# Kernel optimization log

Measured on AMD Instinct MI355X. Metric: run time of the kernel, lower is better.

The kernel has to match this reference:

```python
import jax, jax.numpy as jnp
import numpy as np

B, N, M = 4, 1024, 1024
PFD, AD, GFD = 1024, 256, 512
H, DH = 4, 64
NR, CUT = 16, 2.0
SCALE = DH ** -0.5
OFFSETS = jnp.linspace(0.0, CUT, NR)
COEFF = -0.5 / (CUT / (NR - 1)) ** 2


def _ln(x, g, b, eps=1e-5):
    mu = x.mean(-1, keepdims=True)
    var = ((x - mu) ** 2).mean(-1, keepdims=True)
    return (x - mu) / jnp.sqrt(var + eps) * g + b


def _kabsch(src, tgt, w):
    # weighted Kabsch: rotation/translation aligning src -> tgt
    w = w / (w.sum(-1, keepdims=True) + 1e-8)  # (B,N)
    cs = jnp.einsum('bn,bnc->bc', w, src)
    ct = jnp.einsum('bn,bnc->bc', w, tgt)
    sc = src - cs[:, None]
    tc = tgt - ct[:, None]
    Hm = jnp.einsum('bn,bnc,bnd->bcd', w, sc, tc)  # (B,3,3)
    U, _, Vt = jnp.linalg.svd(Hm)
    V = jnp.swapaxes(Vt, -1, -2)
    d = jnp.linalg.det(V @ jnp.swapaxes(U, -1, -2))
    D = jnp.stack([jnp.ones_like(d), jnp.ones_like(d), d], -1)  # (B,3)
    R = jnp.einsum('bij,bj,bkj->bik', V, D, U)
    t = ct - jnp.einsum('bij,bj->bi', R, cs)
    return R, t


def setup_inputs():
    key = jax.random.key(0)
    it = iter(jax.random.split(key, 48))
    nrm = lambda s, sc=1.0: jax.random.normal(next(it), s, jnp.float32) * sc
    return {
        'src_point_feats': nrm((B, N, PFD)),
        'tgt_point_feats': nrm((B, M, PFD)),
        'src_points': nrm((B, N, 3)),
        'tgt_points': nrm((B, M, 3)),
        'tgt_global': nrm((B, GFD)),
        'sfp_w': nrm((PFD, AD), 0.02), 'sfp_b': jnp.zeros((AD,)), 'sfp_g': jnp.ones((AD,)), 'sfp_bb': jnp.zeros((AD,)),
        'tfp_w': nrm((PFD, AD), 0.02), 'tfp_b': jnp.zeros((AD,)), 'tfp_g': jnp.ones((AD,)), 'tfp_bb': jnp.zeros((AD,)),
        'rbf_w': nrm((NR, H), 0.1),
        'qw': nrm((AD, AD), 0.02), 'qb': jnp.zeros((AD,)),
        'kw': nrm((AD, AD), 0.02), 'kb': jnp.zeros((AD,)),
        'vw': nrm((AD, AD), 0.02), 'vb': jnp.zeros((AD,)),
        'ow': nrm((AD, AD), 0.02), 'ob': jnp.zeros((AD,)),
        'n1_g': jnp.ones((AD,)), 'n1_b': jnp.zeros((AD,)),
        'f1_w': nrm((AD, 4 * AD), 0.02), 'f1_b': jnp.zeros((4 * AD,)),
        'f2_w': nrm((4 * AD, AD), 0.02), 'f2_b': jnp.zeros((AD,)),
        'n2_g': jnp.ones((AD,)), 'n2_b': jnp.zeros((AD,)),
        'scp_w': nrm((AD, AD), 0.02), 'scp_b': jnp.zeros((AD,)),
        'tcp_w': nrm((AD, AD), 0.02), 'tcp_b': jnp.zeros((AD,)),
        'temperature': jnp.array(0.05, jnp.float32),
        'gp_w': nrm((AD, GFD), 0.02), 'gp_b': jnp.zeros((GFD,)), 'gp_g': jnp.ones((GFD,)), 'gp_bb': jnp.zeros((GFD,)),
    }


def reference(src_point_feats, tgt_point_feats, src_points, tgt_points, tgt_global,
              sfp_w, sfp_b, sfp_g, sfp_bb, tfp_w, tfp_b, tfp_g, tfp_bb, rbf_w,
              qw, qb, kw, kb, vw, vb, ow, ob, n1_g, n1_b,
              f1_w, f1_b, f2_w, f2_b, n2_g, n2_b,
              scp_w, scp_b, tcp_w, tcp_b, temperature,
              gp_w, gp_b, gp_g, gp_bb):
    # feature projections
    src_proj = jax.nn.relu(_ln(src_point_feats @ sfp_w + sfp_b, sfp_g, sfp_bb))  # (B,N,AD)
    tgt_proj = jax.nn.relu(_ln(tgt_point_feats @ tfp_w + tfp_b, tfp_g, tfp_bb))  # (B,M,AD)
    # inter-cloud geometric bias: cdist -> gaussian RBF -> per-head linear (dist no-grad)
    d2 = ((src_points ** 2).sum(-1)[:, :, None] + (tgt_points ** 2).sum(-1)[:, None, :]
          - 2.0 * jnp.einsum('bnc,bmc->bnm', src_points, tgt_points))
    dist = jnp.sqrt(jnp.clip(d2, 0.0))  # (B,N,M)
    rbf = jnp.exp(COEFF * (dist[..., None] - OFFSETS) ** 2)  # (B,N,M,NR)
    rbf = jax.lax.stop_gradient(rbf)
    bias = jnp.einsum('bnmr,rh->bhnm', rbf, rbf_w)
    # cross attention with geo bias (pre-LN on both streams, shared LN params)
    xq = _ln(src_proj, n1_g, n1_b)
    xc = _ln(tgt_proj, n1_g, n1_b)
    q = (xq @ qw + qb).reshape(B, N, H, DH)
    k = (xc @ kw + kb).reshape(B, M, H, DH)
    v = (xc @ vw + vb).reshape(B, M, H, DH)
    logits = jnp.einsum('bnhd,bmhd->bhnm', q, k) * SCALE + bias
    p = jax.nn.softmax(logits, axis=-1)
    attn_out = jnp.einsum('bhnm,bmhd->bnhd', p, v).reshape(B, N, AD) @ ow + ob
    x = src_proj + attn_out
    # FFN block (exact GELU as in torch)
    h = _ln(x, n2_g, n2_b)
    x = x + (jax.nn.gelu(h @ f1_w + f1_b, approximate=False) @ f2_w + f2_b)
    # soft correspondences + 3-step log-domain Sinkhorn
    src_corr = x @ scp_w + scp_b
    tgt_corr = tgt_proj @ tcp_w + tcp_b
    tau = jnp.clip(temperature, 0.01, 1.0)
    logS = jnp.einsum('bnd,bmd->bnm', src_corr, tgt_corr) / tau
    for _ in range(3):
        logS = logS - jax.nn.logsumexp(logS, axis=-1, keepdims=True)
        logS = logS - jax.nn.logsumexp(logS, axis=-2, keepdims=True)
    S = jnp.exp(logS)
    tgt_corr_points = jnp.einsum('bnm,bmc->bnc', S, tgt_points)
    confidence = S.max(-1)
    R_res, t_res = _kabsch(src_points, tgt_corr_points, confidence)
    src_global_new = jax.nn.relu(_ln(x.max(1) @ gp_w + gp_b, gp_g, gp_bb))
    combined = jnp.concatenate([src_global_new, tgt_global], axis=-1)
    return R_res, t_res, combined, confidence, S
```

## Files before the change

kernel.cpp:

```cpp
#include <hip/hip_runtime.h>
#include <hip/hip_bf16.h>
#include <math.h>

constexpr int Bn  = 4;
constexpr int Nn  = 1024;
constexpr int Mmm = 1024;
constexpr int PFDc = 1024;
constexpr int ADc  = 256;
constexpr int GFDc = 512;
constexpr int Hc   = 4;
constexpr int NRc  = 16;
constexpr int NSPLIT = 32;
constexpr float COEFFc = -28.125f;
constexpr float SCALEc = 0.125f;
constexpr float STEPc  = 2.0f / 15.0f;

__device__ __forceinline__ float addf(float a, float b) { return a + b; }
__device__ __forceinline__ double addd(double a, double b) { return a + b; }

#define BLK_REDUCE_F(OP, VAR, RES) \
  red[tid] = (VAR); __syncthreads(); \
  for (int st_ = 128; st_ > 0; st_ >>= 1) { if (tid < st_) red[tid] = OP(red[tid], red[tid + st_]); __syncthreads(); } \
  (RES) = red[0]; __syncthreads();

#define BLK_REDUCE_D(OP, VAR, RES) \
  redd[tid] = (VAR); __syncthreads(); \
  for (int st_ = 128; st_ > 0; st_ >>= 1) { if (tid < st_) redd[tid] = OP(redd[tid], redd[tid + st_]); __syncthreads(); } \
  (RES) = redd[0]; __syncthreads();

__device__ __forceinline__ void g512core(
    const float* __restrict__ A, int lda, const float* __restrict__ W, int ldw,
    int kbeg, int kend, int r0, int c0, int tid,
    float As[2][16][68], float Ws[2][16][68], float acc[2][4])
{
  const int tx = tid & 15, ty = tid >> 4;
  float ra[2], rb[2];
  #pragma unroll
  for (int j = 0; j < 2; ++j) {
    int e = tid + j * 512;
    ra[j] = A[(size_t)(r0 + (e >> 4)) * lda + kbeg + (e & 15)];
    rb[j] = W[(size_t)(kbeg + (e >> 6)) * ldw + c0 + (e & 63)];
  }
  #pragma unroll
  for (int j = 0; j < 2; ++j) {
    int e = tid + j * 512;
    As[0][e & 15][e >> 4] = ra[j];
    Ws[0][e >> 6][e & 63] = rb[j];
  }
  __syncthreads();

  const int nstep = (kend - kbeg) >> 4;
  for (int s = 0; s < nstep; ++s) {
    const int cur = s & 1;
    if (s + 1 < nstep) {
      const int k0 = kbeg + ((s + 1) << 4);
      #pragma unroll
      for (int j = 0; j < 2; ++j) {
        int e = tid + j * 512;
        ra[j] = A[(size_t)(r0 + (e >> 4)) * lda + k0 + (e & 15)];
        rb[j] = W[(size_t)(k0 + (e >> 6)) * ldw + c0 + (e & 63)];
      }
    }
    #pragma unroll
    for (int kk = 0; kk < 16; ++kk) {
      float2 av = *(const float2*)&As[cur][kk][ty * 2];
      float4 wv = *(const float4*)&Ws[cur][kk][tx * 4];
      float a[2] = {av.x, av.y};
      float w[4] = {wv.x, wv.y, wv.z, wv.w};
      #pragma unroll
      for (int i = 0; i < 2; ++i)
        #pragma unroll
        for (int j = 0; j < 4; ++j)
          acc[i][j] = fmaf(a[i], w[j], acc[i][j]);
    }
    if (s + 1 < nstep) {
      #pragma unroll
      for (int j = 0; j < 2; ++j) {
        int e = tid + j * 512;
        As[cur ^ 1][e & 15][e >> 4] = ra[j];
        Ws[cur ^ 1][e >> 6][e & 63] = rb[j];
      }
    }
    __syncthreads();
  }
}

__global__ __launch_bounds__(512) void gemm512_k(
    const float* __restrict__ A, const float* __restrict__ W, const float* __restrict__ bias,
    const float* __restrict__ addsrc, float* __restrict__ C,
    int K, int Cc, int act)
{
  __shared__ __align__(16) float As[2][16][68];
  __shared__ __align__(16) float Ws[2][16][68];
  const int tid = threadIdx.x;
  const int tx = tid & 15, ty = tid >> 4;
  const int r0 = blockIdx.y * 64, c0 = blockIdx.x * 64;
  float acc[2][4] = {};
  g512core(A, K, W, Cc, 0, K, r0, c0, tid, As, Ws, acc);
  #pragma unroll
  for (int i = 0; i < 2; ++i) {
    int r = r0 + ty * 2 + i;
    #pragma unroll
    for (int j = 0; j < 4; ++j) {
      int c = c0 + tx * 4 + j;
      float v = acc[i][j] + bias[c];
      if (addsrc) v += addsrc[(size_t)r * Cc + c];
      if (act == 1) v = 0.5f * v * (1.f + erff(v * 0.70710678118654752f));
      C[(size_t)r * Cc + c] = v;
    }
  }
}

__global__ __launch_bounds__(512) void gemm_sk512_k(
    const float* __restrict__ A, const float* __restrict__ W, float* __restrict__ P)
{
  __shared__ __align__(16) float As[2][16][68];
  __shared__ __align__(16) float Ws[2][16][68];
  const int tid = threadIdx.x;
  const int tx = tid & 15, ty = tid >> 4;
  const int r0 = blockIdx.y * 64, c0 = blockIdx.x * 64;
  const int koff = blockIdx.z * 256;
  float acc[2][4] = {};
  g512core(A, 1024, W, 256, koff, koff + 256, r0, c0, tid, As, Ws, acc);
  float* Pz = P + (size_t)blockIdx.z * 1048576;
  #pragma unroll
  for (int i = 0; i < 2; ++i) {
    int r = r0 + ty * 2 + i;
    #pragma unroll
    for (int j = 0; j < 4; ++j)
      Pz[(size_t)r * 256 + c0 + tx * 4 + j] = acc[i][j];
  }
}

__global__ __launch_bounds__(512) void gemm_corr2_k(
    const float* __restrict__ A0, const float* __restrict__ W0, const float* __restrict__ b0,
    float* __restrict__ C0,
    const float* __restrict__ A1, const float* __restrict__ W1, const float* __restrict__ b1,
    float* __restrict__ C1)
{
  __shared__ __align__(16) float As[2][16][68];
  __shared__ __align__(16) float Ws[2][16][68];
  const int tid = threadIdx.x;
  const int tx = tid & 15, ty = tid >> 4;
  const int r0 = blockIdx.y * 64, c0 = blockIdx.x * 64;
  const float* A = blockIdx.z ? A1 : A0;
  const float* W = blockIdx.z ? W1 : W0;
  const float* bias = blockIdx.z ? b1 : b0;
  float* C = blockIdx.z ? C1 : C0;
  float acc[2][4] = {};
  g512core(A, 256, W, 256, 0, 256, r0, c0, tid, As, Ws, acc);
  #pragma unroll
  for (int i = 0; i < 2; ++i) {
    int r = r0 + ty * 2 + i;
    #pragma unroll
    for (int j = 0; j < 4; ++j) {
      int c = c0 + tx * 4 + j;
      C[(size_t)r * 256 + c] = acc[i][j] + bias[c];
    }
  }
}

__global__ __launch_bounds__(256) void gemm_k(
    const float* __restrict__ A, const float* __restrict__ W, const float* __restrict__ bias,
    const float* __restrict__ addsrc, float* __restrict__ C,
    int R, int K, int Cc, int act)
{
  __shared__ __align__(16) float As[16][68];
  __shared__ __align__(16) float Ws[16][68];
  const int tid = threadIdx.x;
  const int tx = tid & 15, ty = tid >> 4;
  const int r0 = blockIdx.y * 64, c0 = blockIdx.x * 64;
  float acc[4][4] = {};
  for (int k0 = 0; k0 < K; k0 += 16) {
    #pragma unroll
    for (int j = 0; j < 4; ++j) {
      int e = tid + j * 256;
      int ar = e >> 4, ak = e & 15;
      int gr = r0 + ar;
      As[ak][ar] = (gr < R) ? A[(size_t)gr * K + k0 + ak] : 0.f;
    }
    #pragma unroll
    for (int j = 0; j < 4; ++j) {
      int e = tid + j * 256;
      int wk = e >> 6, wc = e & 63;
      int gc = c0 + wc;
      Ws[wk][wc] = (gc < Cc) ? W[(size_t)(k0 + wk) * Cc + gc] : 0.f;
    }
    __syncthreads();
    #pragma unroll
    for (int kk = 0; kk < 16; ++kk) {
      float4 av = *(const float4*)&As[kk][ty * 4];
      float4 wv = *(const float4*)&Ws[kk][tx * 4];
      float a[4] = {av.x, av.y, av.z, av.w};
      float w[4] = {wv.x, wv.y, wv.z, wv.w};
      #pragma unroll
      for (int i = 0; i < 4; ++i)
        #pragma unroll
        for (int j = 0; j < 4; ++j)
          acc[i][j] = fmaf(a[i], w[j], acc[i][j]);
    }
    __syncthreads();
  }
  #pragma unroll
  for (int i = 0; i < 4; ++i) {
    int r = r0 + ty * 4 + i;
    if (r >= R) continue;
    #pragma unroll
    for (int j = 0; j < 4; ++j) {
      int c = c0 + tx * 4 + j;
      if (c >= Cc) continue;
      float v = acc[i][j] + bias[c];
      if (addsrc) v += addsrc[(size_t)r * Cc + c];
      if (act == 1) v = 0.5f * v * (1.f + erff(v * 0.70710678118654752f));
      C[(size_t)r * Cc + c] = v;
    }
  }
}

__global__ __launch_bounds__(256) void gemm256_k(
    const float* __restrict__ A, const float* __restrict__ W, const float* __restrict__ bias,
    const float* __restrict__ addsrc, float* __restrict__ C,
    int R, int K, int Cc, int act)
{
  __shared__ __align__(16) float As[2][16][68];
  __shared__ __align__(16) float Ws[2][16][68];
  const int tid = threadIdx.x;
  const int tx = tid & 15, ty = tid >> 4;
  const int r0 = blockIdx.y * 64, c0 = blockIdx.x * 64;
  float acc[4][4] = {};
  float ra[4], rb[4];

  #pragma unroll
  for (int j = 0; j < 4; ++j) {
    int e = tid + j * 256;
    ra[j] = A[(size_t)(r0 + (e >> 4)) * K + (e & 15)];
    rb[j] = W[(size_t)(e >> 6) * Cc + c0 + (e & 63)];
  }
  #pragma unroll
  for (int j = 0; j < 4; ++j) {
    int e = tid + j * 256;
    As[0][e & 15][e >> 4] = ra[j];
    Ws[0][e >> 6][e & 63] = rb[j];
  }
  __syncthreads();

  const int nstep = K >> 4;
  for (int s = 0; s < nstep; ++s) {
    const int cur = s & 1;
    if (s + 1 < nstep) {
      const int k0 = (s + 1) << 4;
      #pragma unroll
      for (int j = 0; j < 4; ++j) {
        int e = tid + j * 256;
        ra[j] = A[(size_t)(r0 + (e >> 4)) * K + k0 + (e & 15)];
        rb[j] = W[(size_t)(k0 + (e >> 6)) * Cc + c0 + (e & 63)];
      }
    }
    #pragma unroll
    for (int kk = 0; kk < 16; ++kk) {
      float4 av = *(const float4*)&As[cur][kk][ty * 4];
      float4 wv = *(const float4*)&Ws[cur][kk][tx * 4];
      float a[4] = {av.x, av.y, av.z, av.w};
      float w[4] = {wv.x, wv.y, wv.z, wv.w};
      #pragma unroll
      for (int i = 0; i < 4; ++i)
        #pragma unroll
        for (int j = 0; j < 4; ++j)
          acc[i][j] = fmaf(a[i], w[j], acc[i][j]);
    }
    if (s + 1 < nstep) {
      #pragma unroll
      for (int j = 0; j < 4; ++j) {
        int e = tid + j * 256;
        As[cur ^ 1][e & 15][e >> 4] = ra[j];
        Ws[cur ^ 1][e >> 6][e & 63] = rb[j];
      }
    }
    __syncthreads();
  }
  #pragma unroll
  for (int i = 0; i < 4; ++i) {
    int r = r0 + ty * 4 + i;
    #pragma unroll
    for (int j = 0; j < 4; ++j) {
      int c = c0 + tx * 4 + j;
      float v = acc[i][j] + bias[c];
      if (addsrc) v += addsrc[(size_t)r * Cc + c];
      if (act == 1) v = 0.5f * v * (1.f + erff(v * 0.70710678118654752f));
      C[(size_t)r * Cc + c] = v;
    }
  }
}

__global__ __launch_bounds__(256) void ln4_k(
    const float* __restrict__ p, const float* __restrict__ bias,
    const float* __restrict__ g, const float* __restrict__ bb,
    float* __restrict__ out, int relu)
{
  const int row = blockIdx.x;
  const int tid = threadIdx.x;
  size_t o = (size_t)row * 256 + tid;
  float x = p[o] + p[o + 1048576] + p[o + 2097152] + p[o + 3145728] + bias[tid];
  float s = x, s2 = x * x;
  #pragma unroll
  for (int off = 32; off > 0; off >>= 1) {
    s  += __shfl_xor(s, off, 64);
    s2 += __shfl_xor(s2, off, 64);
  }
  __shared__ float as_[4], as2_[4];
  const int wv = tid >> 6, ln = tid & 63;
  if (ln == 0) { as_[wv] = s; as2_[wv] = s2; }
  __syncthreads();
  s  = as_[0] + as_[1] + as_[2] + as_[3];
  s2 = as2_[0] + as2_[1] + as2_[2] + as2_[3];
  float mu = s * (1.f / 256.f);
  float var = fmaxf(s2 * (1.f / 256.f) - mu * mu, 0.f);
  float inv = 1.f / sqrtf(var + 1e-5f);
  float v = (x - mu) * inv * g[tid] + bb[tid];
  if (relu) v = fmaxf(v, 0.f);
  out[o] = v;
}

__global__ __launch_bounds__(256) void red4_k(
    const float* __restrict__ p, const float* __restrict__ bias, float* __restrict__ out)
{
  size_t i = (size_t)blockIdx.x * 256 + threadIdx.x;
  out[i] += p[i] + p[i + 1048576] + p[i + 2097152] + p[i + 3145728] + bias[threadIdx.x];
}

__global__ __launch_bounds__(256) void pack_kv_k(
    const float* __restrict__ kw, const float* __restrict__ kb,
    const float* __restrict__ vw, const float* __restrict__ vb,
    float* __restrict__ kvw, float* __restrict__ kvb)
{
  int i = blockIdx.x * 256 + threadIdx.x;
  if (i < 256 * 512) {
    int r = i >> 9, c = i & 511;
    kvw[i] = (c < 256) ? kw[r * 256 + c] : vw[r * 256 + (c - 256)];
  } else if (i < 256 * 512 + 512) {
    int c = i - 256 * 512;
    kvb[c] = (c < 256) ? kb[c] : vb[c - 256];
  }
}

__global__ __launch_bounds__(256) void gemm_nt256_k(
    const float* __restrict__ A, const float* __restrict__ Bm, float* __restrict__ C,
    const float* __restrict__ temp)
{
  const int K = ADc;
  __shared__ __align__(16) float As[2][16][68];
  __shared__ __align__(16) float Bs[2][16][68];
  const int tid = threadIdx.x;
  const int tx = tid & 15, ty = tid >> 4;
  const int b = blockIdx.z;
  const int r0 = blockIdx.y * 64, c0 = blockIdx.x * 64;
  const float* Ab = A + (size_t)b * Nn * K;
  const float* Bb = Bm + (size_t)b * Mmm * K;
  float* Cb = C + (size_t)b * Nn * Mmm;
  float tau = fminf(fmaxf(temp[0], 0.01f), 1.0f);
  float inv_tau = 1.f / tau;
  float acc[4][4] = {};
  float ra[4], rb[4];

  #pragma unroll
  for (int j = 0; j < 4; ++j) {
    int e = tid + j * 256;
    ra[j] = Ab[(size_t)(r0 + (e >> 4)) * K + (e & 15)];
    rb[j] = Bb[(size_t)(c0 + (e >> 4)) * K + (e & 15)];
  }
  #pragma unroll
  for (int j = 0; j < 4; ++j) {
    int e = tid + j * 256;
    As[0][e & 15][e >> 4] = ra[j];
    Bs[0][e & 15][e >> 4] = rb[j];
  }
  __syncthreads();

  for (int s = 0; s < 16; ++s) {
    const int cur = s & 1;
    if (s + 1 < 16) {
      const int k0 = (s + 1) << 4;
      #pragma unroll
      for (int j = 0; j < 4; ++j) {
        int e = tid + j * 256;
        ra[j] = Ab[(size_t)(r0 + (e >> 4)) * K + k0 + (e & 15)];
        rb[j] = Bb[(size_t)(c0 + (e >> 4)) * K + k0 + (e & 15)];
      }
    }
    #pragma unroll
    for (int kk = 0; kk < 16; ++kk) {
      float4 av = *(const float4*)&As[cur][kk][ty * 4];
      float4 wv = *(const float4*)&Bs[cur][kk][tx * 4];
      float a[4] = {av.x, av.y, av.z, av.w};
      float w[4] = {wv.x, wv.y, wv.z, wv.w};
      #pragma unroll
      for (int i = 0; i < 4; ++i)
        #pragma unroll
        for (int j = 0; j < 4; ++j)
          acc[i][j] = fmaf(a[i], w[j], acc[i][j]);
    }
    if (s + 1 < 16) {
      #pragma unroll
      for (int j = 0; j < 4; ++j) {
        int e = tid + j * 256;
        As[cur ^ 1][e & 15][e >> 4] = ra[j];
        Bs[cur ^ 1][e & 15][e >> 4] = rb[j];
      }
    }
    __syncthreads();
  }
  #pragma unroll
  for (int i = 0; i < 4; ++i) {
    int r = r0 + ty * 4 + i;
    #pragma unroll
    for (int j = 0; j < 4; ++j) {
      int c = c0 + tx * 4 + j;
      Cb[(size_t)r * Mmm + c] = acc[i][j] * inv_tau;
    }
  }
}

__global__ __launch_bounds__(256) void ln_k(
    const float* __restrict__ in, const float* __restrict__ g, const float* __restrict__ bb,
    float* __restrict__ out, int Cc, int relu)
{
  const int tid = threadIdx.x;
  const int row = blockIdx.x;
  const float* x = in + (size_t)row * Cc;
  float* o = out + (size_t)row * Cc;
  __shared__ float red[256];
  float s = 0.f;
  for (int j = tid; j < Cc; j += 256) s += x[j];
  float tot; BLK_REDUCE_F(addf, s, tot);
  float mu = tot / Cc;
  float s2 = 0.f;
  for (int j = tid; j < Cc; j += 256) { float d = x[j] - mu; s2 += d * d; }
  float tot2; BLK_REDUCE_F(addf, s2, tot2);
  float inv = 1.f / sqrtf(tot2 / Cc + 1e-5f);
  for (int j = tid; j < Cc; j += 256) {
    float v = (x[j] - mu) * inv * g[j] + bb[j];
    if (relu) v = fmaxf(v, 0.f);
    o[j] = v;
  }
}

__device__ __forceinline__ void ln2_body(
    const float* __restrict__ in, const float* __restrict__ g, const float* __restrict__ bb,
    float* __restrict__ out, int row, int tid, int relu)
{
  float x = in[(size_t)row * 256 + tid];
  float s = x, s2 = x * x;
  #pragma unroll
  for (int off = 32; off > 0; off >>= 1) {
    s  += __shfl_xor(s, off, 64);
    s2 += __shfl_xor(s2, off, 64);
  }
  __shared__ float as_[4], as2_[4];
  const int wv = tid >> 6, ln = tid & 63;
  if (ln == 0) { as_[wv] = s; as2_[wv] = s2; }
  __syncthreads();
  s  = as_[0] + as_[1] + as_[2] + as_[3];
  s2 = as2_[0] + as2_[1] + as2_[2] + as2_[3];
  float mu = s * (1.f / 256.f);
  float var = fmaxf(s2 * (1.f / 256.f) - mu * mu, 0.f);
  float inv = 1.f / sqrtf(var + 1e-5f);
  float v = (x - mu) * inv * g[tid] + bb[tid];
  if (relu) v = fmaxf(v, 0.f);
  out[(size_t)row * 256 + tid] = v;
}

__global__ __launch_bounds__(256) void ln2_k(
    const float* __restrict__ in, const float* __restrict__ g, const float* __restrict__ bb,
    float* __restrict__ out, int relu)
{
  ln2_body(in, g, bb, out, blockIdx.x, threadIdx.x, relu);
}

__global__ __launch_bounds__(256) void ln2x2_k(
    const float* __restrict__ in0, float* __restrict__ out0,
    const float* __restrict__ in1, float* __restrict__ out1,
    const float* __restrict__ g, const float* __restrict__ bb)
{
  const int row = blockIdx.x;
  if (row < Bn * Nn) ln2_body(in0, g, bb, out0, row, threadIdx.x, 0);
  else               ln2_body(in1, g, bb, out1, row - Bn * Nn, threadIdx.x, 0);
}

__global__ __launch_bounds__(256) void fattn(
    const float* __restrict__ q, const float* __restrict__ kv,
    const float* __restrict__ src_pts, const float* __restrict__ tgt_pts,
    const float* __restrict__ rbfw, float* __restrict__ ctx)
{
  const int bh = blockIdx.x;
  const int b = bh >> 2, h = bh & 3;
  const int n0 = blockIdx.y * 32;
  const int tid = threadIdx.x;
  const int tx = tid & 15, ty = tid >> 4;
  const int lane = tid & 63, w = tid >> 6;
  const int mml = lane >> 4;
  const int dd  = lane & 15;

  __shared__ __align__(16) float Qs[64][36];
  __shared__ __align__(16) float Ks[64][68];
  __shared__ __align__(16) float Vs[64][68];
  __shared__ __align__(16) float Ps[32][68];
  __shared__ float spx[32], spy[32], spz[32];
  __shared__ float tpx[64], tpy[64], tpz[64];
  __shared__ float rw[16];
  __shared__ __align__(8) float2 Tb[2048];

  if (tid < 16) rw[tid] = rbfw[tid * Hc + h];
  #pragma unroll
  for (int c = 0; c < 8; ++c) {
    int n = c * 4 + mml;
    int d = w * 16 + dd;
    Qs[d][n] = q[((size_t)b * Nn + n0 + n) * ADc + h * 64 + d];
  }
  if (tid < 32) {
    spx[tid] = src_pts[((size_t)b * Nn + n0 + tid) * 3 + 0];
    spy[tid] = src_pts[((size_t)b * Nn + n0 + tid) * 3 + 1];
    spz[tid] = src_pts[((size_t)b * Nn + n0 + tid) * 3 + 2];
  }
  __syncthreads();

  for (int i = tid; i < 2048; i += 256) {
    float di = (float)i * (1.0f / 512.0f);
    float s0 = 0.f, s1 = 0.f;
    #pragma unroll
    for (int r = 0; r < NRc; ++r) {
      float dq0 = di - STEPc * r;
      float dq1 = dq0 + (1.0f / 512.0f);
      s0 = fmaf(__expf(COEFFc * dq0 * dq0), rw[r], s0);
      s1 = fmaf(__expf(COEFFc * dq1 * dq1), rw[r], s1);
    }
    Tb[i] = make_float2(s0, s1 - s0);
  }

  float kreg[16], vreg[16];
  float tp0 = 0.f, tp1 = 0.f, tp2 = 0.f;
  {
    const size_t kb_ = ((size_t)b * Mmm) * 512 + h * 64;
    #pragma unroll
    for (int c = 0; c < 16; ++c) {
      kreg[c] = kv[kb_ + (size_t)(c * 4 + mml) * 512 + w * 16 + dd];
      vreg[c] = kv[kb_ + (size_t)(c * 4 + w) * 512 + 256 + lane];
    }
    if (tid < 64) {
      tp0 = tgt_pts[((size_t)b * Mmm + tid) * 3 + 0];
      tp1 = tgt_pts[((size_t)b * Mmm + tid) * 3 + 1];
      tp2 = tgt_pts[((size_t)b * Mmm + tid) * 3 + 2];
    }
  }

  float O[2][4] = {};
  float mrun[2] = {-1e30f, -1e30f};
  float lrun[2] = {0.f, 0.f};

  for (int t = 0; t < Mmm / 64; ++t) {
    __syncthreads();
    #pragma unroll
    for (int c = 0; c < 16; ++c) Ks[w * 16 + dd][c * 4 + mml] = kreg[c];
    #pragma unroll
    for (int c = 0; c < 16; ++c) Vs[c * 4 + w][lane] = vreg[c];
    if (tid < 64) { tpx[tid] = tp0; tpy[tid] = tp1; tpz[tid] = tp2; }
    if (t + 1 < Mmm / 64) {
      const size_t kb_ = ((size_t)b * Mmm + (t + 1) * 64) * 512 + h * 64;
      #pragma unroll
      for (int c = 0; c < 16; ++c) {
        kreg[c] = kv[kb_ + (size_t)(c * 4 + mml) * 512 + w * 16 + dd];
        vreg[c] = kv[kb_ + (size_t)(c * 4 + w) * 512 + 256 + lane];
      }
// ... 305 lines not shown
  for (int r = 0; r < 3; ++r) { vv[0][r] = V[r][i0]; vv[1][r] = V[r][i1]; vv[2][r] = V[r][i2]; }
  double sg[3] = { sqrt(fmax(lam[i0], 0.0)), sqrt(fmax(lam[i1], 0.0)), sqrt(fmax(lam[i2], 0.0)) };

  double uu[3][3];
  double eps = 1e-12 * (sg[0] > 0 ? sg[0] : 1.0);
  if (sg[0] > eps) {
    for (int r = 0; r < 3; ++r)
      uu[0][r] = (A[r][0] * vv[0][0] + A[r][1] * vv[0][1] + A[r][2] * vv[0][2]) / sg[0];
    double n = sqrt(uu[0][0]*uu[0][0] + uu[0][1]*uu[0][1] + uu[0][2]*uu[0][2]);
    if (n > 1e-14) { uu[0][0]/=n; uu[0][1]/=n; uu[0][2]/=n; }
  } else { uu[0][0]=1; uu[0][1]=0; uu[0][2]=0; }
  if (sg[1] > eps) {
    for (int r = 0; r < 3; ++r)
      uu[1][r] = (A[r][0] * vv[1][0] + A[r][1] * vv[1][1] + A[r][2] * vv[1][2]) / sg[1];
  } else {
    int ax = (fabs(uu[0][0]) <= fabs(uu[0][1]) && fabs(uu[0][0]) <= fabs(uu[0][2])) ? 0
           : (fabs(uu[0][1]) <= fabs(uu[0][2]) ? 1 : 2);
    uu[1][0] = uu[1][1] = uu[1][2] = 0.0; uu[1][ax] = 1.0;
  }
  {
    double pr = uu[0][0]*uu[1][0] + uu[0][1]*uu[1][1] + uu[0][2]*uu[1][2];
    for (int r = 0; r < 3; ++r) uu[1][r] -= pr * uu[0][r];
    double n = sqrt(uu[1][0]*uu[1][0] + uu[1][1]*uu[1][1] + uu[1][2]*uu[1][2]);
    if (n > 1e-14) { uu[1][0]/=n; uu[1][1]/=n; uu[1][2]/=n; }
  }
  if (sg[2] > eps) {
    for (int r = 0; r < 3; ++r)
      uu[2][r] = (A[r][0] * vv[2][0] + A[r][1] * vv[2][1] + A[r][2] * vv[2][2]) / sg[2];
    double p0 = uu[0][0]*uu[2][0] + uu[0][1]*uu[2][1] + uu[0][2]*uu[2][2];
    double p1 = uu[1][0]*uu[2][0] + uu[1][1]*uu[2][1] + uu[1][2]*uu[2][2];
    for (int r = 0; r < 3; ++r) uu[2][r] -= p0 * uu[0][r] + p1 * uu[1][r];
    double n = sqrt(uu[2][0]*uu[2][0] + uu[2][1]*uu[2][1] + uu[2][2]*uu[2][2]);
    if (n > 1e-14) { uu[2][0]/=n; uu[2][1]/=n; uu[2][2]/=n; }
    else {
      uu[2][0] = uu[0][1]*uu[1][2] - uu[0][2]*uu[1][1];
      uu[2][1] = uu[0][2]*uu[1][0] - uu[0][0]*uu[1][2];
      uu[2][2] = uu[0][0]*uu[1][1] - uu[0][1]*uu[1][0];
    }
  } else {
    uu[2][0] = uu[0][1]*uu[1][2] - uu[0][2]*uu[1][1];
    uu[2][1] = uu[0][2]*uu[1][0] - uu[0][0]*uu[1][2];
    uu[2][2] = uu[0][0]*uu[1][1] - uu[0][1]*uu[1][0];
  }

  double detU = trip(uu[0], uu[1], uu[2]);
  double detV = trip(vv[0], vv[1], vv[2]);
  double d = (detU * detV < 0.0) ? -1.0 : 1.0;

  double R[3][3];
  for (int i = 0; i < 3; ++i)
    for (int j = 0; j < 3; ++j)
      R[i][j] = vv[0][i] * uu[0][j] + vv[1][i] * uu[1][j] + d * vv[2][i] * uu[2][j];
  for (int i = 0; i < 3; ++i) {
    double t = ct[i] - (R[i][0] * cs[0] + R[i][1] * cs[1] + R[i][2] * cs[2]);
    outT[(size_t)b * 3 + i] = (float)t;
    for (int j = 0; j < 3; ++j)
      outR[(size_t)b * 9 + i * 3 + j] = (float)R[i][j];
  }
}

__global__ __launch_bounds__(256) void xmax_part_k(const float* __restrict__ x, float* __restrict__ part)
{
  const int b = blockIdx.x, ch = blockIdx.y;
  const int d = threadIdx.x;
  float mx = -1e30f;
  const int n0 = ch * 64;
  for (int n = n0; n < n0 + 64; ++n)
    mx = fmaxf(mx, x[((size_t)b * Nn + n) * ADc + d]);
  part[((size_t)b * 16 + ch) * ADc + d] = mx;
}

__global__ __launch_bounds__(256) void xmax_comb_k(const float* __restrict__ part, float* __restrict__ xmax)
{
  const int b = blockIdx.x, d = threadIdx.x;
  float mx = -1e30f;
  for (int c = 0; c < 16; ++c) mx = fmaxf(mx, part[((size_t)b * 16 + c) * ADc + d]);
  xmax[(size_t)b * ADc + d] = mx;
}

__global__ __launch_bounds__(256) void combined_k(
    const float* __restrict__ gl, const float* __restrict__ tgt_global, float* __restrict__ outC)
{
  int i = blockIdx.x * 256 + threadIdx.x;
  int b = i >> 10, j = i & 1023;
  float v = (j < GFDc) ? gl[(size_t)b * GFDc + j] : tgt_global[(size_t)b * GFDc + (j - GFDc)];
  outC[i] = v;
}

extern "C" void kernel_launch(void* const* d_in, const int* in_sizes, int n_in,
                              void* d_out, int out_size, void* d_ws, size_t ws_size,
                              hipStream_t stream) {
  (void)in_sizes; (void)n_in; (void)out_size; (void)ws_size;
  const float* src_feats = (const float*)d_in[0];
  const float* tgt_feats = (const float*)d_in[1];
  const float* src_pts   = (const float*)d_in[2];
  const float* tgt_pts   = (const float*)d_in[3];
  const float* tgt_glob  = (const float*)d_in[4];
  const float* sfp_w = (const float*)d_in[5];  const float* sfp_b = (const float*)d_in[6];
  const float* sfp_g = (const float*)d_in[7];  const float* sfp_bb = (const float*)d_in[8];
  const float* tfp_w = (const float*)d_in[9];  const float* tfp_b = (const float*)d_in[10];
  const float* tfp_g = (const float*)d_in[11]; const float* tfp_bb = (const float*)d_in[12];
  const float* rbf_w = (const float*)d_in[13];
  const float* qw = (const float*)d_in[14]; const float* qb = (const float*)d_in[15];
  const float* kw = (const float*)d_in[16]; const float* kb = (const float*)d_in[17];
  const float* vw = (const float*)d_in[18]; const float* vb = (const float*)d_in[19];
  const float* ow = (const float*)d_in[20]; const float* ob = (const float*)d_in[21];
  const float* n1_g = (const float*)d_in[22]; const float* n1_b = (const float*)d_in[23];
  const float* f1_w = (const float*)d_in[24]; const float* f1_b = (const float*)d_in[25];
  const float* f2_w = (const float*)d_in[26]; const float* f2_b = (const float*)d_in[27];
  const float* n2_g = (const float*)d_in[28]; const float* n2_b = (const float*)d_in[29];
  const float* scp_w = (const float*)d_in[30]; const float* scp_b = (const float*)d_in[31];
  const float* tcp_w = (const float*)d_in[32]; const float* tcp_b = (const float*)d_in[33];
  const float* temp  = (const float*)d_in[34];
  const float* gp_w = (const float*)d_in[35]; const float* gp_b = (const float*)d_in[36];
  const float* gp_g = (const float*)d_in[37]; const float* gp_bb = (const float*)d_in[38];

  float* out = (float*)d_out;
  float* outR    = out;
  float* outT    = out + 36;
  float* outC    = out + 48;
  float* outConf = out + 48 + 4096;
  float* outS    = out + 48 + 4096 + 4096;

  float* ws = (float*)d_ws;
  const size_t M1 = 1048576;
  float* A_   = ws + 0 * M1;
  float* B_   = ws + 1 * M1;
  float* C_   = ws + 2 * M1;
  float* D_   = ws + 3 * M1;
  float* E_   = ws + 4 * M1;
  float* F_   = ws + 5 * M1;
  float* G_   = ws + 6 * M1;
  float* logS = ws + 0 * M1;
  float* hid  = ws + 1 * M1;
  float* tail = ws + 7 * M1;
  float* colLse = tail;
  float* pmax   = colLse + 4096;
  float* psum   = pmax + 131072;
  float* conf   = psum + 131072;
  float* tcp    = conf + 4096;
  float* xmax   = tcp + 12288;
  float* glraw  = xmax + 1024;
  float* gl     = glraw + 2048;
  double* kab   = (double*)(gl + 2048);
  float* xpart  = (float*)(kab + 64);
  float* Rn     = xpart + 16384;
  float* kvw    = pmax;
  float* kvb    = psum;

  const int BN = Bn * Nn;

  pack_kv_k<<<514, 256, 0, stream>>>(kw, kb, vw, vb, kvw, kvb);

  gemm_sk512_k<<<dim3(4, 64, 4), 512, 0, stream>>>(src_feats, sfp_w, outS);
  ln4_k<<<BN, 256, 0, stream>>>(outS, sfp_b, sfp_g, sfp_bb, G_, 1);
  gemm_sk512_k<<<dim3(4, 64, 4), 512, 0, stream>>>(tgt_feats, tfp_w, outS);
  ln4_k<<<BN, 256, 0, stream>>>(outS, tfp_b, tfp_g, tfp_bb, F_, 1);

  ln2x2_k<<<2 * BN, 256, 0, stream>>>(G_, A_, F_, B_, n1_g, n1_b);
  gemm512_k<<<dim3(4, 64), 512, 0, stream>>>(A_, qw, qb, nullptr, C_, ADc, ADc, 0);
  gemm512_k<<<dim3(8, 64), 512, 0, stream>>>(B_, kvw, kvb, nullptr, D_, ADc, 512, 0);

  fattn<<<dim3(Bn * Hc, Nn / 32), 256, 0, stream>>>(C_, D_, src_pts, tgt_pts, rbf_w, B_);
  gemm512_k<<<dim3(4, 64), 512, 0, stream>>>(B_, ow, ob, G_, G_, ADc, ADc, 0);

  ln2_k<<<BN, 256, 0, stream>>>(G_, n2_g, n2_b, A_, 0);
  gemm256_k<<<dim3(16, 64), 256, 0, stream>>>(A_, f1_w, f1_b, nullptr, hid, BN, ADc, 1024, 1);
  gemm_sk512_k<<<dim3(4, 64, 4), 512, 0, stream>>>(hid, f2_w, outS);
  red4_k<<<BN, 256, 0, stream>>>(outS, f2_b, G_);

  gemm_corr2_k<<<dim3(4, 64, 2), 512, 0, stream>>>(G_, scp_w, scp_b, E_,
                                                   F_, tcp_w, tcp_b, outS);
  gemm_nt256_k<<<dim3(16, 16, Bn), 256, 0, stream>>>(E_, outS, logS, temp);

  for (int it = 0; it < 3; ++it) {
    row_lse3_k<<<BN, 256, 0, stream>>>(logS, it == 0 ? nullptr : colLse, Rn);
    col_part2_k<<<dim3(Mmm / 256, NSPLIT, Bn), 256, 0, stream>>>(logS, Rn, pmax, psum);
    col_comb_k<<<dim3(Mmm / 256, Bn), 256, 0, stream>>>(pmax, psum, colLse);
  }
  finalize2_k<<<BN, 256, 0, stream>>>(logS, Rn, colLse, tgt_pts, outS, outConf, conf, tcp);

  kabsch_red_k<<<Bn, 256, 0, stream>>>(conf, src_pts, tcp, kab);
  kabsch_svd_k<<<1, 64, 0, stream>>>(kab, outR, outT);

  xmax_part_k<<<dim3(Bn, 16), 256, 0, stream>>>(G_, xpart);
  xmax_comb_k<<<Bn, 256, 0, stream>>>(xpart, xmax);
  gemm_k<<<dim3(GFDc / 64, 1), 256, 0, stream>>>(xmax, gp_w, gp_b, nullptr, glraw, Bn, ADc, GFDc, 0);
  ln_k<<<Bn, 256, 0, stream>>>(glraw, gp_g, gp_bb, gl, GFDc, 1);
  combined_k<<<(Bn * 2 * GFDc) / 256, 256, 0, stream>>>(gl, tgt_glob, outC);
}
```

Before: 741.8 us.

## Use 128x128 register-blocked tiles for large GEMMs and fuse the dual projections

Replaces the 64x64 tiled GEMMs used for the feature projections, the FFN and the similarity matrix with 128x128 tiles, where each of 512 threads computes an 8x4 output block. This raises arithmetic intensity per shared-memory load and cuts global reloads. The src and tgt split-K projections now run as one launch, and their LayerNorm reductions are also merged into one kernel, using the hid buffer as scratch. The cost is fewer blocks per GEMM (128-256), which may underfill the GPU's compute units, plus higher register pressure.

```diff
diff --git a/kernel.cpp b/kernel.cpp
--- a/kernel.cpp
+++ b/kernel.cpp
@@ -28,6 +28,213 @@
   for (int st_ = 128; st_ > 0; st_ >>= 1) { if (tid < st_) redd[tid] = OP(redd[tid], redd[tid + st_]); __syncthreads(); } \
   (RES) = redd[0]; __syncthreads();
 
+__device__ __forceinline__ void g128core(
+    const float* __restrict__ A, int lda, const float* __restrict__ W, int ldw,
+    int kbeg, int kend, int r0, int c0, int tid,
+    float As[2][8][132], float Ws[2][8][132], float acc[8][4])
+{
+  const int tx = tid & 31, ty = tid >> 5;
+  float ra[2], rb[2];
+  #pragma unroll
+  for (int j = 0; j < 2; ++j) {
+    int e = tid + j * 512;
+    ra[j] = A[(size_t)(r0 + (e >> 3)) * lda + kbeg + (e & 7)];
+    rb[j] = W[(size_t)(kbeg + (e >> 7)) * ldw + c0 + (e & 127)];
+  }
+  #pragma unroll
+  for (int j = 0; j < 2; ++j) {
+    int e = tid + j * 512;
+    As[0][e & 7][e >> 3] = ra[j];
+    Ws[0][e >> 7][e & 127] = rb[j];
+  }
+  __syncthreads();
+
+  const int nstep = (kend - kbeg) >> 3;
+  for (int s = 0; s < nstep; ++s) {
+    const int cur = s & 1;
+    if (s + 1 < nstep) {
+      const int k0 = kbeg + ((s + 1) << 3);
+      #pragma unroll
+      for (int j = 0; j < 2; ++j) {
+        int e = tid + j * 512;
+        ra[j] = A[(size_t)(r0 + (e >> 3)) * lda + k0 + (e & 7)];
+        rb[j] = W[(size_t)(k0 + (e >> 7)) * ldw + c0 + (e & 127)];
+      }
+    }
+    #pragma unroll
+    for (int kk = 0; kk < 8; ++kk) {
+      float4 a0 = *(const float4*)&As[cur][kk][ty * 4];
+      float4 a1 = *(const float4*)&As[cur][kk][64 + ty * 4];
+      float2 w0 = *(const float2*)&Ws[cur][kk][tx * 2];
+      float2 w1 = *(const float2*)&Ws[cur][kk][64 + tx * 2];
+      float a[8] = {a0.x, a0.y, a0.z, a0.w, a1.x, a1.y, a1.z, a1.w};
+      float w[4] = {w0.x, w0.y, w1.x, w1.y};
+      #pragma unroll
+      for (int i = 0; i < 8; ++i)
+        #pragma unroll
+        for (int j = 0; j < 4; ++j)
+          acc[i][j] = fmaf(a[i], w[j], acc[i][j]);
+    }
+    if (s + 1 < nstep) {
+      #pragma unroll
+      for (int j = 0; j < 2; ++j) {
+        int e = tid + j * 512;
+        As[cur ^ 1][e & 7][e >> 3] = ra[j];
+        Ws[cur ^ 1][e >> 7][e & 127] = rb[j];
+      }
+    }
+    __syncthreads();
+  }
+}
+
+__device__ __forceinline__ int g128row(int i, int ty) { return (i < 4) ? ty * 4 + i : 64 + ty * 4 + (i - 4); }
+__device__ __forceinline__ int g128col(int j, int tx) { return (j < 2) ? tx * 2 + j : 64 + tx * 2 + (j - 2); }
+
+__global__ __launch_bounds__(512) void gemm128_k(
+    const float* __restrict__ A, const float* __restrict__ W, const float* __restrict__ bias,
+    float* __restrict__ C, int K, int Cc, int act)
+{
+  __shared__ __align__(16) float As[2][8][132];
+  __shared__ __align__(16) float Ws[2][8][132];
+  const int tid = threadIdx.x;
+  const int tx = tid & 31, ty = tid >> 5;
+  const int r0 = blockIdx.y * 128, c0 = blockIdx.x * 128;
+  float acc[8][4] = {};
+  g128core(A, K, W, Cc, 0, K, r0, c0, tid, As, Ws, acc);
+  #pragma unroll
+  for (int i = 0; i < 8; ++i) {
+    int r = r0 + g128row(i, ty);
+    #pragma unroll
+    for (int j = 0; j < 4; ++j) {
+      int c = c0 + g128col(j, tx);
+      float v = acc[i][j] + bias[c];
+      if (act == 1) v = 0.5f * v * (1.f + erff(v * 0.70710678118654752f));
+      C[(size_t)r * Cc + c] = v;
+    }
+  }
+}
+
+__global__ __launch_bounds__(512) void gemm128sk_k(
+    const float* __restrict__ A, const float* __restrict__ W, float* __restrict__ P)
+{
+  __shared__ __align__(16) float As[2][8][132];
+  __shared__ __align__(16) float Ws[2][8][132];
+  const int tid = threadIdx.x;
+  const int tx = tid & 31, ty = tid >> 5;
+  const int r0 = blockIdx.y * 128, c0 = blockIdx.x * 128;
+  const int koff = blockIdx.z * 256;
+  float acc[8][4] = {};
+  g128core(A, 1024, W, 256, koff, koff + 256, r0, c0, tid, As, Ws, acc);
+  float* Pz = P + (size_t)blockIdx.z * 1048576;
+  #pragma unroll
+  for (int i = 0; i < 8; ++i) {
+    int r = r0 + g128row(i, ty);
+    #pragma unroll
+    for (int j = 0; j < 4; ++j)
+      Pz[(size_t)r * 256 + c0 + g128col(j, tx)] = acc[i][j];
+  }
+}
+
+__global__ __launch_bounds__(512) void proj2sk_k(
+    const float* __restrict__ srcf, const float* __restrict__ sfw,
+    const float* __restrict__ tgtf, const float* __restrict__ tfw,
+    float* __restrict__ Psrc, float* __restrict__ Ptgt)
+{
+  __shared__ __align__(16) float As[2][8][132];
+  __shared__ __align__(16) float Ws[2][8][132];
+  const int tid = threadIdx.x;
+  const int tx = tid & 31, ty = tid >> 5;
+  const int z = blockIdx.z;
+  const float* A = (z < 4) ? srcf : tgtf;
+  const float* W = (z < 4) ? sfw : tfw;
+  float* P = ((z < 4) ? Psrc : Ptgt) + (size_t)(z & 3) * 1048576;
+  const int r0 = blockIdx.y * 128, c0 = blockIdx.x * 128;
+  const int koff = (z & 3) * 256;
+  float acc[8][4] = {};
+  g128core(A, 1024, W, 256, koff, koff + 256, r0, c0, tid, As, Ws, acc);
+  #pragma unroll
+  for (int i = 0; i < 8; ++i) {
+    int r = r0 + g128row(i, ty);
+    #pragma unroll
+    for (int j = 0; j < 4; ++j)
+      P[(size_t)r * 256 + c0 + g128col(j, tx)] = acc[i][j];
+  }
+}
+
+__global__ __launch_bounds__(512) void gemm128nt_k(
+    const float* __restrict__ A, const float* __restrict__ Bm, float* __restrict__ C,
+    const float* __restrict__ temp)
+{
+  __shared__ __align__(16) float As[2][8][132];
+  __shared__ __align__(16) float Bs[2][8][132];
+  const int tid = threadIdx.x;
+  const int tx = tid & 31, ty = tid >> 5;
+  const int b = blockIdx.z;
+  const int r0 = blockIdx.y * 128, c0 = blockIdx.x * 128;
+  const float* Ab = A + (size_t)b * Nn * ADc;
+  const float* Bb = Bm + (size_t)b * Mmm * ADc;
+  float* Cb = C + (size_t)b * Nn * Mmm;
+  float tau = fminf(fmaxf(temp[0], 0.01f), 1.0f);
+  float inv_tau = 1.f / tau;
+  float acc[8][4] = {};
+  float ra[2], rb[2];
+  #pragma unroll
+  for (int j = 0; j < 2; ++j) {
+    int e = tid + j * 512;
+    ra[j] = Ab[(size_t)(r0 + (e >> 3)) * ADc + (e & 7)];
+    rb[j] = Bb[(size_t)(c0 + (e >> 3)) * ADc + (e & 7)];
+  }
+  #pragma unroll
+  for (int j = 0; j < 2; ++j) {
+    int e = tid + j * 512;
+    As[0][e & 7][e >> 3] = ra[j];
+    Bs[0][e & 7][e >> 3] = rb[j];
+  }
+  __syncthreads();
+  for (int s = 0; s < 32; ++s) {
+    const int cur = s & 1;
+    if (s + 1 < 32) {
+      const int k0 = (s + 1) << 3;
+      #pragma unroll
+      for (int j = 0; j < 2; ++j) {
+        int e = tid + j * 512;
+        ra[j] = Ab[(size_t)(r0 + (e >> 3)) * ADc + k0 + (e & 7)];
+        rb[j] = Bb[(size_t)(c0 + (e >> 3)) * ADc + k0 + (e & 7)];
+      }
+    }
+    #pragma unroll
+    for (int kk = 0; kk < 8; ++kk) {
+      float4 a0 = *(const float4*)&As[cur][kk][ty * 4];
+      float4 a1 = *(const float4*)&As[cur][kk][64 + ty * 4];
+      float2 w0 = *(const float2*)&Bs[cur][kk][tx * 2];
+      float2 w1 = *(const float2*)&Bs[cur][kk][64 + tx * 2];
+      float a[8] = {a0.x, a0.y, a0.z, a0.w, a1.x, a1.y, a1.z, a1.w};
+      float w[4] = {w0.x, w0.y, w1.x, w1.y};
+      #pragma unroll
+      for (int i = 0; i < 8; ++i)
+        #pragma unroll
+        for (int j = 0; j < 4; ++j)
+          acc[i][j] = fmaf(a[i], w[j], acc[i][j]);
+    }
+    if (s + 1 < 32) {
+      #pragma unroll
+      for (int j = 0; j < 2; ++j) {
+        int e = tid + j * 512;
+        As[cur ^ 1][e & 7][e >> 3] = ra[j];
+        Bs[cur ^ 1][e & 7][e >> 3] = rb[j];
+      }
+    }
+    __syncthreads();
+  }
+  #pragma unroll
+  for (int i = 0; i < 8; ++i) {
+    int r = r0 + g128row(i, ty);
+    #pragma unroll
+    for (int j = 0; j < 4; ++j)
+      Cb[(size_t)r * Mmm + c0 + g128col(j, tx)] = acc[i][j] * inv_tau;
+  }
+}
+
 __device__ __forceinline__ void g512core(
     const float* __restrict__ A, int lda, const float* __restrict__ W, int ldw,
     int kbeg, int kend, int r0, int c0, int tid,
@@ -108,27 +315,6 @@
       if (act == 1) v = 0.5f * v * (1.f + erff(v * 0.70710678118654752f));
       C[(size_t)r * Cc + c] = v;
     }
-  }
-}
-
-__global__ __launch_bounds__(512) void gemm_sk512_k(
-    const float* __restrict__ A, const float* __restrict__ W, float* __restrict__ P)
-{
-  __shared__ __align__(16) float As[2][16][68];
-  __shared__ __align__(16) float Ws[2][16][68];
-  const int tid = threadIdx.x;
-  const int tx = tid & 15, ty = tid >> 4;
-  const int r0 = blockIdx.y * 64, c0 = blockIdx.x * 64;
-  const int koff = blockIdx.z * 256;
-  float acc[2][4] = {};
-  g512core(A, 1024, W, 256, koff, koff + 256, r0, c0, tid, As, Ws, acc);
-  float* Pz = P + (size_t)blockIdx.z * 1048576;
-  #pragma unroll
-  for (int i = 0; i < 2; ++i) {
-    int r = r0 + ty * 2 + i;
-    #pragma unroll
-    for (int j = 0; j < 4; ++j)
-      Pz[(size_t)r * 256 + c0 + tx * 4 + j] = acc[i][j];
   }
 }
 
@@ -217,88 +403,11 @@
   }
 }
 
-__global__ __launch_bounds__(256) void gemm256_k(
-    const float* __restrict__ A, const float* __restrict__ W, const float* __restrict__ bias,
-    const float* __restrict__ addsrc, float* __restrict__ C,
-    int R, int K, int Cc, int act)
-{
-  __shared__ __align__(16) float As[2][16][68];
-  __shared__ __align__(16) float Ws[2][16][68];
-  const int tid = threadIdx.x;
-  const int tx = tid & 15, ty = tid >> 4;
-  const int r0 = blockIdx.y * 64, c0 = blockIdx.x * 64;
-  float acc[4][4] = {};
-  float ra[4], rb[4];
-
-  #pragma unroll
-  for (int j = 0; j < 4; ++j) {
-    int e = tid + j * 256;
-    ra[j] = A[(size_t)(r0 + (e >> 4)) * K + (e & 15)];
-    rb[j] = W[(size_t)(e >> 6) * Cc + c0 + (e & 63)];
-  }
-  #pragma unroll
-  for (int j = 0; j < 4; ++j) {
-    int e = tid + j * 256;
-    As[0][e & 15][e >> 4] = ra[j];
-    Ws[0][e >> 6][e & 63] = rb[j];
-  }
-  __syncthreads();
-
-  const int nstep = K >> 4;
-  for (int s = 0; s < nstep; ++s) {
-    const int cur = s & 1;
-    if (s + 1 < nstep) {
-      const int k0 = (s + 1) << 4;
-      #pragma unroll
-      for (int j = 0; j < 4; ++j) {
-        int e = tid + j * 256;
-        ra[j] = A[(size_t)(r0 + (e >> 4)) * K + k0 + (e & 15)];
-        rb[j] = W[(size_t)(k0 + (e >> 6)) * Cc + c0 + (e & 63)];
-      }
-    }
-    #pragma unroll
-    for (int kk = 0; kk < 16; ++kk) {
-      float4 av = *(const float4*)&As[cur][kk][ty * 4];
-      float4 wv = *(const float4*)&Ws[cur][kk][tx * 4];
-      float a[4] = {av.x, av.y, av.z, av.w};
-      float w[4] = {wv.x, wv.y, wv.z, wv.w};
-      #pragma unroll
-      for (int i = 0; i < 4; ++i)
-        #pragma unroll
-        for (int j = 0; j < 4; ++j)
-          acc[i][j] = fmaf(a[i], w[j], acc[i][j]);
-    }
-    if (s + 1 < nstep) {
-      #pragma unroll
-      for (int j = 0; j < 4; ++j) {
-        int e = tid + j * 256;
-        As[cur ^ 1][e & 15][e >> 4] = ra[j];
-        Ws[cur ^ 1][e >> 6][e & 63] = rb[j];
-      }
-    }
-    __syncthreads();
-  }
-  #pragma unroll
-  for (int i = 0; i < 4; ++i) {
-    int r = r0 + ty * 4 + i;
-    #pragma unroll
-    for (int j = 0; j < 4; ++j) {
-      int c = c0 + tx * 4 + j;
-      float v = acc[i][j] + bias[c];
-      if (addsrc) v += addsrc[(size_t)r * Cc + c];
-      if (act == 1) v = 0.5f * v * (1.f + erff(v * 0.70710678118654752f));
-      C[(size_t)r * Cc + c] = v;
-    }
-  }
-}
-
-__global__ __launch_bounds__(256) void ln4_k(
+__device__ __forceinline__ void ln4_body(
     const float* __restrict__ p, const float* __restrict__ bias,
     const float* __restrict__ g, const float* __restrict__ bb,
-    float* __restrict__ out, int relu)
-{
-  const int row = blockIdx.x;
-  const int tid = threadIdx.x;
+    float* __restrict__ out, int row, int tid)
+{
   size_t o = (size_t)row * 256 + tid;
   float x = p[o] + p[o + 1048576] + p[o + 2097152] + p[o + 3145728] + bias[tid];
   float s = x, s2 = x * x;
@@ -317,8 +426,18 @@
   float var = fmaxf(s2 * (1.f / 256.f) - mu * mu, 0.f);
   float inv = 1.f / sqrtf(var + 1e-5f);
   float v = (x - mu) * inv * g[tid] + bb[tid];
-  if (relu) v = fmaxf(v, 0.f);
-  out[o] = v;
+  out[o] = fmaxf(v, 0.f);
+}
+
+__global__ __launch_bounds__(256) void ln4x2_k(
+    const float* __restrict__ p0, const float* __restrict__ b0,
+    const float* __restrict__ g0, const float* __restrict__ bb0, float* __restrict__ o0,
+    const float* __restrict__ p1, const float* __restrict__ b1,
+    const float* __restrict__ g1, const float* __restrict__ bb1, float* __restrict__ o1)
+{
+  const int row = blockIdx.x;
+  if (row < Bn * Nn) ln4_body(p0, b0, g0, bb0, o0, row, threadIdx.x);
+  else               ln4_body(p1, b1, g1, bb1, o1, row - Bn * Nn, threadIdx.x);
 }
 
 __global__ __launch_bounds__(256) void red4_k(
@@ -340,83 +459,6 @@
   } else if (i < 256 * 512 + 512) {
     int c = i - 256 * 512;
     kvb[c] = (c < 256) ? kb[c] : vb[c - 256];
-  }
-}
-
-__global__ __launch_bounds__(256) void gemm_nt256_k(
-    const float* __restrict__ A, const float* __restrict__ Bm, float* __restrict__ C,
-    const float* __restrict__ temp)
-{
-  const int K = ADc;
-  __shared__ __align__(16) float As[2][16][68];
-  __shared__ __align__(16) float Bs[2][16][68];
-  const int tid = threadIdx.x;
-  const int tx = tid & 15, ty = tid >> 4;
-  const int b = blockIdx.z;
-  const int r0 = blockIdx.y * 64, c0 = blockIdx.x * 64;
-  const float* Ab = A + (size_t)b * Nn * K;
-  const float* Bb = Bm + (size_t)b * Mmm * K;
-  float* Cb = C + (size_t)b * Nn * Mmm;
-  float tau = fminf(fmaxf(temp[0], 0.01f), 1.0f);
-  float inv_tau = 1.f / tau;
-  float acc[4][4] = {};
-  float ra[4], rb[4];
-
-  #pragma unroll
-  for (int j = 0; j < 4; ++j) {
-    int e = tid + j * 256;
-    ra[j] = Ab[(size_t)(r0 + (e >> 4)) * K + (e & 15)];
-    rb[j] = Bb[(size_t)(c0 + (e >> 4)) * K + (e & 15)];
-  }
-  #pragma unroll
-  for (int j = 0; j < 4; ++j) {
-    int e = tid + j * 256;
-    As[0][e & 15][e >> 4] = ra[j];
-    Bs[0][e & 15][e >> 4] = rb[j];
-  }
-  __syncthreads();
-
-  for (int s = 0; s < 16; ++s) {
-    const int cur = s & 1;
-    if (s + 1 < 16) {
-      const int k0 = (s + 1) << 4;
-      #pragma unroll
-      for (int j = 0; j < 4; ++j) {
-        int e = tid + j * 256;
-        ra[j] = Ab[(size_t)(r0 + (e >> 4)) * K + k0 + (e & 15)];
-        rb[j] = Bb[(size_t)(c0 + (e >> 4)) * K + k0 + (e & 15)];
-      }
-    }
-    #pragma unroll
-    for (int kk = 0; kk < 16; ++kk) {
-      float4 av = *(const float4*)&As[cur][kk][ty * 4];
-      float4 wv = *(const float4*)&Bs[cur][kk][tx * 4];
-      float a[4] = {av.x, av.y, av.z, av.w};
-      float w[4] = {wv.x, wv.y, wv.z, wv.w};
-      #pragma unroll
-      for (int i = 0; i < 4; ++i)
-        #pragma unroll
-        for (int j = 0; j < 4; ++j)
-          acc[i][j] = fmaf(a[i], w[j], acc[i][j]);
-    }
-    if (s + 1 < 16) {
-      #pragma unroll
-      for (int j = 0; j < 4; ++j) {
-        int e = tid + j * 256;
-        As[cur ^ 1][e & 15][e >> 4] = ra[j];
-        Bs[cur ^ 1][e & 15][e >> 4] = rb[j];
-      }
-    }
-    __syncthreads();
-  }
-  #pragma unroll
-  for (int i = 0; i < 4; ++i) {
-    int r = r0 + ty * 4 + i;
-    #pragma unroll
-    for (int j = 0; j < 4; ++j) {
-      int c = c0 + tx * 4 + j;
-      Cb[(size_t)r * Mmm + c] = acc[i][j] * inv_tau;
-    }
   }
 }
 
@@ -1028,10 +1070,9 @@
 
   pack_kv_k<<<514, 256, 0, stream>>>(kw, kb, vw, vb, kvw, kvb);
 
-  gemm_sk512_k<<<dim3(4, 64, 4), 512, 0, stream>>>(src_feats, sfp_w, outS);
-  ln4_k<<<BN, 256, 0, stream>>>(outS, sfp_b, sfp_g, sfp_bb, G_, 1);
-  gemm_sk512_k<<<dim3(4, 64, 4), 512, 0, stream>>>(tgt_feats, tfp_w, outS);
-  ln4_k<<<BN, 256, 0, stream>>>(outS, tfp_b, tfp_g, tfp_bb, F_, 1);
+  proj2sk_k<<<dim3(2, 32, 8), 512, 0, stream>>>(src_feats, sfp_w, tgt_feats, tfp_w, outS, hid);
+  ln4x2_k<<<2 * BN, 256, 0, stream>>>(outS, sfp_b, sfp_g, sfp_bb, G_,
+                                      hid, tfp_b, tfp_g, tfp_bb, F_);
 
   ln2x2_k<<<2 * BN, 256, 0, stream>>>(G_, A_, F_, B_, n1_g, n1_b);
   gemm512_k<<<dim3(4, 64), 512, 0, stream>>>(A_, qw, qb, nullptr, C_, ADc, ADc, 0);
@@ -1041,13 +1082,13 @@
   gemm512_k<<<dim3(4, 64), 512, 0, stream>>>(B_, ow, ob, G_, G_, ADc, ADc, 0);
 
   ln2_k<<<BN, 256, 0, stream>>>(G_, n2_g, n2_b, A_, 0);
-  gemm256_k<<<dim3(16, 64), 256, 0, stream>>>(A_, f1_w, f1_b, nullptr, hid, BN, ADc, 1024, 1);
-  gemm_sk512_k<<<dim3(4, 64, 4), 512, 0, stream>>>(hid, f2_w, outS);
+  gemm128_k<<<dim3(8, 32), 512, 0, stream>>>(A_, f1_w, f1_b, hid, ADc, 1024, 1);
+  gemm128sk_k<<<dim3(2, 32, 4), 512, 0, stream>>>(hid, f2_w, outS);
   red4_k<<<BN, 256, 0, stream>>>(outS, f2_b, G_);
 
   gemm_corr2_k<<<dim3(4, 64, 2), 512, 0, stream>>>(G_, scp_w, scp_b, E_,
                                                    F_, tcp_w, tcp_b, outS);
-  gemm_nt256_k<<<dim3(16, 16, Bn), 256, 0, stream>>>(E_, outS, logS, temp);
+  gemm128nt_k<<<dim3(8, 8, Bn), 512, 0, stream>>>(E_, outS, logS, temp);
 
   for (int it = 0; it < 3; ++it) {
     row_lse3_k<<<BN, 256, 0, stream>>>(logS, it == 0 ? nullptr : colLse, Rn);
```

After: 720.6 us. 1.03x faster.
